# Performance work log

Hardware: AMD Instinct MI355X
Metric: run time of the kernel (lower is better)

Reference implementation:

```python
import jax, jax.numpy as jnp
import numpy as np

EPS = 1e-5
GROUPS = 32


def group_norm(x, w, b):
    # x: [N, C]; GroupNorm over 1x1 spatial == per-group norm over C//GROUPS chans
    N, C = x.shape
    xg = x.reshape(N, GROUPS, C // GROUPS)
    mu = xg.mean(-1, keepdims=True)
    var = xg.var(-1, keepdims=True)
    xn = ((xg - mu) * jax.lax.rsqrt(var + EPS)).reshape(N, C)
    return xn * w + b


def rb(x, gn1w, gn1b, c1w, c1b, gn2w, gn2b, c2w, c2b):
    # Conv2d 3x3 pad=1 on a 1x1 spatial input: only the center tap sees data
    # (all other taps hit zero padding), so it reduces exactly to a GEMM with
    # the [out, in] center slice of the kernel.
    h = jax.nn.silu(group_norm(x, gn1w, gn1b))
    h = h @ c1w[:, :, 1, 1].T + c1b
    h = jax.nn.silu(group_norm(h, gn2w, gn2b))
    h = h @ c2w[:, :, 1, 1].T + c2b
    return h + x  # skip == Identity (in_ch == out_ch)


def setup_inputs() -> dict:
    key = jax.random.key(0)
    ks = jax.random.split(key, 20)
    BS, CAND, D, H, W = 32, 2048, 256, 32, 32
    s = 0.05
    inp = {
        "gimage": jax.random.normal(ks[0], (BS, D, H, W), dtype=jnp.float32),
        "pts": jax.random.randint(ks[1], (BS, CAND, 1, 2), 0, 256, dtype=jnp.int32),
        # two stacked RB blocks
        "gn1_w": jnp.ones((2, D), jnp.float32),
        "gn1_b": jnp.zeros((2, D), jnp.float32),
        "conv1_w": jax.random.normal(ks[2], (2, D, D, 3, 3), jnp.float32) * s,
        "conv1_b": jnp.zeros((2, D), jnp.float32),
        "gn2_w": jnp.ones((2, D), jnp.float32),
        "gn2_b": jnp.zeros((2, D), jnp.float32),
        "conv2_w": jax.random.normal(ks[3], (2, D, D, 3, 3), jnp.float32) * s,
        "conv2_b": jnp.zeros((2, D), jnp.float32),
        # class_embed: Linear(256, 2)
        "cls_w": jax.random.normal(ks[4], (2, D), jnp.float32) * s,
        "cls_b": jnp.zeros((2,), jnp.float32),
        # bbox_embed: MLP(256, 256, 4, 3)
        "mlp_w1": jax.random.normal(ks[5], (D, D), jnp.float32) * s,
        "mlp_b1": jnp.zeros((D,), jnp.float32),
        "mlp_w2": jax.random.normal(ks[6], (D, D), jnp.float32) * s,
        "mlp_b2": jnp.zeros((D,), jnp.float32),
        "mlp_w3": jax.random.normal(ks[7], (4, D), jnp.float32) * s,
        "mlp_b3": jnp.zeros((4,), jnp.float32),
    }
    return inp


def reference(gimage, pts, gn1_w, gn1_b, conv1_w, conv1_b, gn2_w, gn2_b,
              conv2_w, conv2_b, cls_w, cls_b, mlp_w1, mlp_b1, mlp_w2, mlp_b2,
              mlp_w3, mlp_b3):
    bs, C, H, W = gimage.shape
    c = pts.shape[1]
    # patch_idx = (pts // 8)[:, :, 0, :] -> (iy, ix) per (batch, candidate)
    idx = pts[:, :, 0, :] // 8                      # [bs, c, 2]
    lin = idx[..., 0] * W + idx[..., 1]             # [bs, c] flat spatial index
    g = gimage.reshape(bs, C, H * W)
    feat = jnp.take_along_axis(g, lin[:, None, :].astype(jnp.int32), axis=2)  # [bs, C, c]
    x = feat.transpose(0, 2, 1).reshape(bs * c, C)  # [(bs c), 256]

    for i in range(2):  # convLayer = Sequential(RB, RB)
        x = rb(x, gn1_w[i], gn1_b[i], conv1_w[i], conv1_b[i],
               gn2_w[i], gn2_b[i], conv2_w[i], conv2_b[i])

    logits = x @ cls_w.T + cls_b                    # [(bs c), 2]
    h = jax.nn.relu(x @ mlp_w1.T + mlp_b1)
    h = jax.nn.relu(h @ mlp_w2.T + mlp_b2)
    boxes = jax.nn.sigmoid(h @ mlp_w3.T + mlp_b3)   # [(bs c), 4]

    pred_logits = logits.reshape(bs, c, 2)
    pred_boxes = boxes.reshape(bs, c, 4)
    return pred_logits, pred_boxes
```

## Files before the change

### kernel.cpp

```cpp
#include <hip/hip_runtime.h>


typedef __attribute__((ext_vector_type(8))) _Float16 half8;
typedef __attribute__((ext_vector_type(4))) float f32x4;

#define AS 264

#define NHALF  393216
#define OFF_WC1 0
#define OFF_WC2 131072
#define OFF_W1  262144
#define OFF_W2  327680
#define WS_NEED 1572864

__device__ __forceinline__ float sigm(float y) { return 1.f / (1.f + __expf(-y)); }

__global__ __launch_bounds__(256) void prep(const float* __restrict__ c1w,
                                            const float* __restrict__ c2w,
                                            const float* __restrict__ w1,
                                            const float* __restrict__ w2,
                                            _Float16* __restrict__ ws) {
  int i = blockIdx.x * 256 + threadIdx.x;
  {
    float v = c1w[(size_t)i * 9 + 4];
    _Float16 h = (_Float16)v;
    ws[OFF_WC1 + i] = h;
    ws[NHALF + OFF_WC1 + i] = (_Float16)(v - (float)h);
  }
  {
    float v = c2w[(size_t)i * 9 + 4];
    _Float16 h = (_Float16)v;
    ws[OFF_WC2 + i] = h;
    ws[NHALF + OFF_WC2 + i] = (_Float16)(v - (float)h);
  }
  if (i < 65536) {
    float v = w1[i];
    _Float16 h = (_Float16)v;
    ws[OFF_W1 + i] = h;
    ws[NHALF + OFF_W1 + i] = (_Float16)(v - (float)h);
    v = w2[i];
    h = (_Float16)v;
    ws[OFF_W2 + i] = h;
    ws[NHALF + OFF_W2 + i] = (_Float16)(v - (float)h);
  }
}

__device__ __forceinline__ void hl_store(_Float16* __restrict__ Ah,
                                         _Float16* __restrict__ Al,
                                         int idx, float v) {
  _Float16 h = (_Float16)v;
  Ah[idx] = h;
  Al[idx] = (_Float16)(v - (float)h);
}

__device__ __forceinline__ void mfma_run(f32x4 acc[2][4],
    const _Float16* __restrict__ Ah, const _Float16* __restrict__ Al,
    const _Float16* __restrict__ Wh, const _Float16* __restrict__ Wl,
    int aoff, size_t boff) {
  half8 bh[4], bl[4];
  #pragma unroll
  for (int nt = 0; nt < 4; nt++) {
    bh[nt] = *(const half8*)(Wh + boff + (nt << 12));
    bl[nt] = *(const half8*)(Wl + boff + (nt << 12));
  }
  #pragma unroll
  for (int mt = 0; mt < 2; mt++)
    #pragma unroll
    for (int nt = 0; nt < 4; nt++)
      acc[mt][nt] = (f32x4){0.f, 0.f, 0.f, 0.f};
  __syncthreads();
  #pragma unroll
  for (int kt = 0; kt < 8; kt++) {
    half8 ah0 = *(const half8*)(Ah + aoff + kt * 32);
    half8 ah1 = *(const half8*)(Ah + aoff + 16 * AS + kt * 32);
    half8 al0 = *(const half8*)(Al + aoff + kt * 32);
    half8 al1 = *(const half8*)(Al + aoff + 16 * AS + kt * 32);
    #pragma unroll
    for (int nt = 0; nt < 4; nt++) {
      acc[0][nt] = __builtin_amdgcn_mfma_f32_16x16x32_f16(ah0, bh[nt], acc[0][nt], 0, 0, 0);
      acc[1][nt] = __builtin_amdgcn_mfma_f32_16x16x32_f16(ah1, bh[nt], acc[1][nt], 0, 0, 0);
      acc[0][nt] = __builtin_amdgcn_mfma_f32_16x16x32_f16(ah0, bl[nt], acc[0][nt], 0, 0, 0);
      acc[1][nt] = __builtin_amdgcn_mfma_f32_16x16x32_f16(ah1, bl[nt], acc[1][nt], 0, 0, 0);
      acc[0][nt] = __builtin_amdgcn_mfma_f32_16x16x32_f16(al0, bh[nt], acc[0][nt], 0, 0, 0);
      acc[1][nt] = __builtin_amdgcn_mfma_f32_16x16x32_f16(al1, bh[nt], acc[1][nt], 0, 0, 0);
    }
    if (kt < 7) {
      #pragma unroll
      for (int nt = 0; nt < 4; nt++) {
        bh[nt] = *(const half8*)(Wh + boff + (nt << 12) + (kt + 1) * 32);
        bl[nt] = *(const half8*)(Wl + boff + (nt << 12) + (kt + 1) * 32);
      }
    }
  }
}

__device__ __forceinline__ void gn_x_to_A(const float x[2][4][4],
    const float* __restrict__ gnw, const float* __restrict__ gnb,
    int col, int quad, int nb,
    _Float16* __restrict__ Ah, _Float16* __restrict__ Al) {
  #pragma unroll
  for (int nt = 0; nt < 4; nt++) {
    int n = nb + (nt << 4) + col;
    float gwv = gnw[n], gbv = gnb[n];
    #pragma unroll
    for (int mt = 0; mt < 2; mt++) {
      #pragma unroll
      for (int rg = 0; rg < 4; rg++) {
        float v = x[mt][nt][rg];
        float s = v, q = v * v;
        s += __shfl_xor(s, 1); q += __shfl_xor(q, 1);
        s += __shfl_xor(s, 2); q += __shfl_xor(q, 2);
        s += __shfl_xor(s, 4); q += __shfl_xor(q, 4);
        float mu = s * 0.125f;
        float rs = rsqrtf(q * 0.125f - mu * mu + 1e-5f);
        float y = (v - mu) * rs * gwv + gbv;
        float sv = y * sigm(y);
        hl_store(Ah, Al, ((mt << 4) + (quad << 2) + rg) * AS + n, sv);
      }
    }
  }
}

__device__ __forceinline__ void epi_gn_to_A(const f32x4 acc[2][4],
    const float* __restrict__ bias,
    const float* __restrict__ gnw, const float* __restrict__ gnb,
    int col, int quad, int nb,
    _Float16* __restrict__ Ah, _Float16* __restrict__ Al) {
  #pragma unroll
  for (int nt = 0; nt < 4; nt++) {
    int n = nb + (nt << 4) + col;
    float bv = bias[n];
    float gwv = gnw[n], gbv = gnb[n];
    #pragma unroll
    for (int mt = 0; mt < 2; mt++) {
      #pragma unroll
      for (int rg = 0; rg < 4; rg++) {
        float v = acc[mt][nt][rg] + bv;
        float s = v, q = v * v;
        s += __shfl_xor(s, 1); q += __shfl_xor(q, 1);
        s += __shfl_xor(s, 2); q += __shfl_xor(q, 2);
        s += __shfl_xor(s, 4); q += __shfl_xor(q, 4);
        float mu = s * 0.125f;
        float rs = rsqrtf(q * 0.125f - mu * mu + 1e-5f);
        float y = (v - mu) * rs * gwv + gbv;
        float sv = y * sigm(y);
        hl_store(Ah, Al, ((mt << 4) + (quad << 2) + rg) * AS + n, sv);
      }
    }
  }
}

__device__ __forceinline__ void epi_relu_to_A(const f32x4 acc[2][4],
    const float* __restrict__ bias, int col, int quad, int nb,
    _Float16* __restrict__ Ah, _Float16* __restrict__ Al) {
  #pragma unroll
  for (int nt = 0; nt < 4; nt++) {
    int n = nb + (nt << 4) + col;
    float bv = bias[n];
    #pragma unroll
    for (int mt = 0; mt < 2; mt++)
      #pragma unroll
      for (int rg = 0; rg < 4; rg++)
        hl_store(Ah, Al, ((mt << 4) + (quad << 2) + rg) * AS + n,
                 fmaxf(acc[mt][nt][rg] + bv, 0.f));
  }
}

__global__ __launch_bounds__(256, 4) void fused_mfma(
    const float* __restrict__ gimage, const int* __restrict__ pts,
    const float* __restrict__ gn1w, const float* __restrict__ gn1b,
    const float* __restrict__ c1b,
    const float* __restrict__ gn2w, const float* __restrict__ gn2b,
    const float* __restrict__ c2b,
    const float* __restrict__ clsw, const float* __restrict__ clsb,
    const float* __restrict__ b1, const float* __restrict__ b2,
    const float* __restrict__ w3, const float* __restrict__ b3,
    const _Float16* __restrict__ ws, float* __restrict__ out) {
  __shared__ _Float16 Ah[32 * AS];
  __shared__ _Float16 Al[32 * AS];
  __shared__ float red[4][32][4];

  const int t = threadIdx.x;
  const int w = t >> 6;
  const int lane = t & 63;
  const int col = lane & 15;
  const int quad = lane >> 4;
  const int nb = w << 6;
  const int row0 = blockIdx.x << 5;
  const int rbase = quad << 2;

  const int aoff = col * AS + (quad << 3);
  const size_t boff = (((size_t)(nb + col)) << 8) + (quad << 3);
  const _Float16* wsl = ws + NHALF;

  float x[2][4][4];
  {
    int lin[2][4];
    #pragma unroll
    for (int mt = 0; mt < 2; mt++)
      #pragma unroll
      for (int rg = 0; rg < 4; rg++) {
        int grow = row0 + (mt << 4) + rbase + rg;
        int p0 = pts[2 * grow], p1 = pts[2 * grow + 1];
        lin[mt][rg] = ((p0 >> 3) << 5) + (p1 >> 3);
      }
    const float* gbase = gimage + (((size_t)((row0 >> 11) << 8)) << 10);
    #pragma unroll
    for (int nt = 0; nt < 4; nt++) {
      const float* gc = gbase + (((size_t)(nb + (nt << 4) + col)) << 10);
      #pragma unroll
      for (int mt = 0; mt < 2; mt++)
        #pragma unroll
        for (int rg = 0; rg < 4; rg++)
          x[mt][nt][rg] = gc[lin[mt][rg]];
    }
  }

  f32x4 acc[2][4];

  #pragma unroll 1
  for (int rb = 0; rb < 2; rb++) {
    gn_x_to_A(x, gn1w + (rb << 8), gn1b + (rb << 8), col, quad, nb, Ah, Al);
    mfma_run(acc, Ah, Al, ws + OFF_WC1 + (rb << 16), wsl + OFF_WC1 + (rb << 16),
             aoff, boff);
    __syncthreads();
    epi_gn_to_A(acc, c1b + (rb << 8), gn2w + (rb << 8), gn2b + (rb << 8),
                col, quad, nb, Ah, Al);
    mfma_run(acc, Ah, Al, ws + OFF_WC2 + (rb << 16), wsl + OFF_WC2 + (rb << 16),
             aoff, boff);
    __syncthreads();
    #pragma unroll
    for (int nt = 0; nt < 4; nt++) {
      float bv = c2b[(rb << 8) + nb + (nt << 4) + col];
      #pragma unroll
      for (int mt = 0; mt < 2; mt++)
        #pragma unroll
        for (int rg = 0; rg < 4; rg++)
          x[mt][nt][rg] += acc[mt][nt][rg] + bv;
    }
  }

  #pragma unroll
  for (int nt = 0; nt < 4; nt++) {
    int n = nb + (nt << 4) + col;
    #pragma unroll
    for (int mt = 0; mt < 2; mt++)
      #pragma unroll
      for (int rg = 0; rg < 4; rg++)
        hl_store(Ah, Al, ((mt << 4) + rbase + rg) * AS + n, x[mt][nt][rg]);
  }
  {
    float pc[2][2][4];
    #pragma unroll
    for (int j = 0; j < 2; j++) {
      #pragma unroll
      for (int mt = 0; mt < 2; mt++)
        #pragma unroll
        for (int rg = 0; rg < 4; rg++)
          pc[j][mt][rg] = 0.f;
      #pragma unroll
      for (int nt = 0; nt < 4; nt++) {
        float wv = clsw[(j << 8) + nb + (nt << 4) + col];
        #pragma unroll
        for (int mt = 0; mt < 2; mt++)
          #pragma unroll
          for (int rg = 0; rg < 4; rg++)
            pc[j][mt][rg] += x[mt][nt][rg] * wv;
      }
    }
    #pragma unroll
    for (int j = 0; j < 2; j++)
      #pragma unroll
      for (int mt = 0; mt < 2; mt++)
        #pragma unroll
        for (int rg = 0; rg < 4; rg++) {
          float p = pc[j][mt][rg];
          p += __shfl_xor(p, 1);
          p += __shfl_xor(p, 2);
          p += __shfl_xor(p, 4);
          p += __shfl_xor(p, 8);
          if (col == 0) red[w][(mt << 4) + rbase + rg][j] = p;
        }
  }

  mfma_run(acc, Ah, Al, ws + OFF_W1, wsl + OFF_W1, aoff, boff);
  if (t < 64) {
    int r = t >> 1, j = t & 1;
    out[((size_t)(row0 + r) << 1) + j] =
        clsb[j] + red[0][r][j] + red[1][r][j] + red[2][r][j] + red[3][r][j];
  }
  __syncthreads();
  epi_relu_to_A(acc, b1, col, quad, nb, Ah, Al);

  mfma_run(acc, Ah, Al, ws + OFF_W2, wsl + OFF_W2, aoff, boff);
  __syncthreads();
  {
    float pb[4][2][4];
    #pragma unroll
    for (int j = 0; j < 4; j++)
      #pragma unroll
      for (int mt = 0; mt < 2; mt++)
        #pragma unroll
        for (int rg = 0; rg < 4; rg++)
          pb[j][mt][rg] = 0.f;
    #pragma unroll
    for (int nt = 0; nt < 4; nt++) {
      int n = nb + (nt << 4) + col;
      float bv = b2[n];
      float w0 = w3[n], w1v = w3[256 + n], w2v = w3[512 + n], w3v = w3[768 + n];
      #pragma unroll
      for (int mt = 0; mt < 2; mt++)
        #pragma unroll
        for (int rg = 0; rg < 4; rg++) {
          float v = fmaxf(acc[mt][nt][rg] + bv, 0.f);
          pb[0][mt][rg] += v * w0;
          pb[1][mt][rg] += v * w1v;
          pb[2][mt][rg] += v * w2v;
          pb[3][mt][rg] += v * w3v;
        }
    }
    #pragma unroll
    for (int j = 0; j < 4; j++)
      #pragma unroll
      for (int mt = 0; mt < 2; mt++)
        #pragma unroll
        for (int rg = 0; rg < 4; rg++) {
          float p = pb[j][mt][rg];
          p += __shfl_xor(p, 1);
          p += __shfl_xor(p, 2);
          p += __shfl_xor(p, 4);
          p += __shfl_xor(p, 8);
          if (col == 0) red[w][(mt << 4) + rbase + rg][j] = p;
        }
  }
  __syncthreads();
  if (t < 128) {
    int r = t >> 2, j = t & 3;
    float s = b3[j] + red[0][r][j] + red[1][r][j] + red[2][r][j] + red[3][r][j];
    out[131072 + ((size_t)(row0 + r) << 2) + j] = sigm(s);
  }
}

#define LS 260
template <int EPI, bool CONV>
__device__ __forceinline__ void gemm_f32(const float* __restrict__ src,
                                         const float* __restrict__ W,
                                         const float* __restrict__ bias,
                                         float* __restrict__ dst,
                                         float* __restrict__ X) {
  const int n = threadIdx.x;
  float acc[32];
  #pragma unroll
  for (int r = 0; r < 32; r++) acc[r] = 0.f;
  #pragma unroll 1
  for (int k = 0; k < 256; k += 8) {
    float w[8];
    if (CONV) {
      #pragma unroll
      for (int j = 0; j < 8; j++) w[j] = W[(size_t)((n << 8) + k + j) * 9 + 4];
    } else {
      f32x4 wa = *(const f32x4*)(W + (n << 8) + k);
      f32x4 wb = *(const f32x4*)(W + (n << 8) + k + 4);
      w[0] = wa[0]; w[1] = wa[1]; w[2] = wa[2]; w[3] = wa[3];
      w[4] = wb[0]; w[5] = wb[1]; w[6] = wb[2]; w[7] = wb[3];
    }
    #pragma unroll
    for (int r = 0; r < 32; r++) {
      const float* xr = src + r * LS + k;
      f32x4 a0 = *(const f32x4*)xr, a1 = *(const f32x4*)(xr + 4);
      acc[r] += a0[0] * w[0] + a0[1] * w[1] + a0[2] * w[2] + a0[3] * w[3]
              + a1[0] * w[4] + a1[1] * w[5] + a1[2] * w[6] + a1[3] * w[7];
    }
  }
  float bv = bias[n];
  #pragma unroll
  for (int r = 0; r < 32; r++) {
    float v = acc[r] + bv;
    if (EPI == 0) dst[r * LS + n] = v;
    else if (EPI == 1) X[r * LS + n] += v;
    else dst[r * LS + n] = fmaxf(v, 0.f);
  }
}
__device__ __forceinline__ void gn_silu32(const float* __restrict__ src,
                                          float* __restrict__ dst,
                                          const float* __restrict__ gw,
                                          const float* __restrict__ gb, int t) {
  #pragma unroll
  for (int i = 0; i < 4; i++) {
    int task = (i << 8) + t;
    int r = task >> 5, g = task & 31;
    const float* x = src + r * LS + (g << 3);
    f32x4 x0 = *(const f32x4*)x, x1 = *(const f32x4*)(x + 4);
    float xx[8] = {x0[0], x0[1], x0[2], x0[3], x1[0], x1[1], x1[2], x1[3]};
    float s = 0.f, q = 0.f;
    #pragma unroll
    for (int j = 0; j < 8; j++) { s += xx[j]; q += xx[j] * xx[j]; }
    float mu = s * 0.125f;
    float rs = rsqrtf(q * 0.125f - mu * mu + 1e-5f);
    const float* w = gw + (g << 3);
    const float* b = gb + (g << 3);
    float* d = dst + r * LS + (g << 3);
    #pragma unroll
    for (int j = 0; j < 8; j++) {
      float y = (xx[j] - mu) * rs * w[j] + b[j];
      d[j] = y * sigm(y);
    }
  }
}
__global__ __launch_bounds__(256, 1) void fused_all(
    const float* __restrict__ gimage, const int* __restrict__ pts,
    const float* __restrict__ gn1w, const float* __restrict__ gn1b,
    const float* __restrict__ c1w, const float* __restrict__ c1b,
    const float* __restrict__ gn2w, const float* __restrict__ gn2b,
    const float* __restrict__ c2w, const float* __restrict__ c2b,
    const float* __restrict__ clsw, const float* __restrict__ clsb,
    const float* __restrict__ w1, const float* __restrict__ b1,
    const float* __restrict__ w2, const float* __restrict__ b2,
    const float* __restrict__ w3, const float* __restrict__ b3,
    float* __restrict__ out) {
  __shared__ float X[32 * LS];
  __shared__ float A[32 * LS];
  __shared__ float H[32 * LS];
  const int t = threadIdx.x;
  const int row0 = blockIdx.x << 5;
  {
    int r = t >> 3;
    int c0 = (t & 7) << 5;
    int grow = row0 + r;
    int p0 = pts[2 * grow], p1 = pts[2 * grow + 1];
    int lin = ((p0 >> 3) << 5) + (p1 >> 3);
    int b = grow >> 11;
    const float* src = gimage + (((size_t)((b << 8) + c0)) << 10) + lin;
    #pragma unroll
    for (int c = 0; c < 32; c++) X[r * LS + c0 + c] = src[(size_t)c << 10];
  }
  __syncthreads();
  #pragma unroll 1
  for (int rb = 0; rb < 2; rb++) {
    gn_silu32(X, A, gn1w + (rb << 8), gn1b + (rb << 8), t);
    __syncthreads();
    gemm_f32<0, true>(A, c1w + rb * 589824, c1b + (rb << 8), H, nullptr);
    __syncthreads();
    gn_silu32(H, A, gn2w + (rb << 8), gn2b + (rb << 8), t);
    __syncthreads();
    gemm_f32<1, true>(A, c2w + rb * 589824, c2b + (rb << 8), nullptr, X);
    __syncthreads();
  }
  if (t < 64) {
    int r = t >> 1, j = t & 1;
    float s = clsb[j];
    const float* w = clsw + (j << 8);
    const float* x = X + r * LS;
    #pragma unroll 1
    for (int k = 0; k < 256; k += 4) {
      f32x4 wv = *(const f32x4*)(w + k);
      f32x4 xv = *(const f32x4*)(x + k);
      s += xv[0] * wv[0] + xv[1] * wv[1] + xv[2] * wv[2] + xv[3] * wv[3];
    }
    out[((size_t)(row0 + r) << 1) + j] = s;
  }
  gemm_f32<2, false>(X, w1, b1, H, nullptr);
  __syncthreads();
  gemm_f32<2, false>(H, w2, b2, A, nullptr);
  __syncthreads();
  if (t < 128) {
    int r = t >> 2, j = t & 3;
    float s = b3[j];
    const float* w = w3 + (j << 8);
    const float* x = A + r * LS;
    #pragma unroll 1
    for (int k = 0; k < 256; k += 4) {
      f32x4 wv = *(const f32x4*)(w + k);
      f32x4 xv = *(const f32x4*)(x + k);
      s += xv[0] * wv[0] + xv[1] * wv[1] + xv[2] * wv[2] + xv[3] * wv[3];
    }
    out[131072 + ((size_t)(row0 + r) << 2) + j] = sigm(s);
  }
}

extern "C" void kernel_launch(void* const* d_in, const int* in_sizes, int n_in,
                              void* d_out, int out_size, void* d_ws, size_t ws_size,
                              hipStream_t stream) {
  const float* gimage = (const float*)d_in[0];
  const int* pts = (const int*)d_in[1];
  const float* gn1w = (const float*)d_in[2];
  const float* gn1b = (const float*)d_in[3];
  const float* c1w = (const float*)d_in[4];
  const float* c1b = (const float*)d_in[5];
  const float* gn2w = (const float*)d_in[6];
  const float* gn2b = (const float*)d_in[7];
  const float* c2w = (const float*)d_in[8];
  const float* c2b = (const float*)d_in[9];
  const float* clsw = (const float*)d_in[10];
  const float* clsb = (const float*)d_in[11];
  const float* w1 = (const float*)d_in[12];
  const float* b1 = (const float*)d_in[13];
  const float* w2 = (const float*)d_in[14];
  const float* b2 = (const float*)d_in[15];
  const float* w3 = (const float*)d_in[16];
  const float* b3 = (const float*)d_in[17];

  if (ws_size >= (size_t)WS_NEED) {
    _Float16* ws = (_Float16*)d_ws;
    prep<<<512, 256, 0, stream>>>(c1w, c2w, w1, w2, ws);
    fused_mfma<<<2048, 256, 0, stream>>>(gimage, pts, gn1w, gn1b, c1b,
                                         gn2w, gn2b, c2b, clsw, clsb,
                                         b1, b2, w3, b3, ws, (float*)d_out);
  } else {
    fused_all<<<2048, 256, 0, stream>>>(gimage, pts, gn1w, gn1b, c1w, c1b,
                                        gn2w, gn2b, c2w, c2b, clsw, clsb,
                                        w1, b1, w2, b2, w3, b3, (float*)d_out);
  }
}
```

Baseline: 548.5 us.

## Double rows per block to 64 with 512 threads sharing weight fragments

```diff
diff --git a/kernel.cpp b/kernel.cpp
--- a/kernel.cpp
+++ b/kernel.cpp
@@ -96,7 +96,7 @@
 
 __device__ __forceinline__ void gn_x_to_A(const float x[2][4][4],
     const float* __restrict__ gnw, const float* __restrict__ gnb,
-    int col, int quad, int nb,
+    int col, int quad, int nb, int rh,
     _Float16* __restrict__ Ah, _Float16* __restrict__ Al) {
   #pragma unroll
   for (int nt = 0; nt < 4; nt++) {
@@ -115,7 +115,7 @@
         float rs = rsqrtf(q * 0.125f - mu * mu + 1e-5f);
         float y = (v - mu) * rs * gwv + gbv;
         float sv = y * sigm(y);
-        hl_store(Ah, Al, ((mt << 4) + (quad << 2) + rg) * AS + n, sv);
+        hl_store(Ah, Al, (rh + (mt << 4) + (quad << 2) + rg) * AS + n, sv);
       }
     }
   }
@@ -124,7 +124,7 @@
 __device__ __forceinline__ void epi_gn_to_A(const f32x4 acc[2][4],
     const float* __restrict__ bias,
     const float* __restrict__ gnw, const float* __restrict__ gnb,
-    int col, int quad, int nb,
+    int col, int quad, int nb, int rh,
     _Float16* __restrict__ Ah, _Float16* __restrict__ Al) {
   #pragma unroll
   for (int nt = 0; nt < 4; nt++) {
@@ -144,14 +144,14 @@
         float rs = rsqrtf(q * 0.125f - mu * mu + 1e-5f);
         float y = (v - mu) * rs * gwv + gbv;
         float sv = y * sigm(y);
-        hl_store(Ah, Al, ((mt << 4) + (quad << 2) + rg) * AS + n, sv);
+        hl_store(Ah, Al, (rh + (mt << 4) + (quad << 2) + rg) * AS + n, sv);
       }
     }
   }
 }
 
 __device__ __forceinline__ void epi_relu_to_A(const f32x4 acc[2][4],
-    const float* __restrict__ bias, int col, int quad, int nb,
+    const float* __restrict__ bias, int col, int quad, int nb, int rh,
     _Float16* __restrict__ Ah, _Float16* __restrict__ Al) {
   #pragma unroll
   for (int nt = 0; nt < 4; nt++) {
@@ -161,12 +161,12 @@
     for (int mt = 0; mt < 2; mt++)
       #pragma unroll
       for (int rg = 0; rg < 4; rg++)
-        hl_store(Ah, Al, ((mt << 4) + (quad << 2) + rg) * AS + n,
+        hl_store(Ah, Al, (rh + (mt << 4) + (quad << 2) + rg) * AS + n,
                  fmaxf(acc[mt][nt][rg] + bv, 0.f));
   }
 }
 
-__global__ __launch_bounds__(256, 4) void fused_mfma(
+__global__ __launch_bounds__(512, 3) void fused_mfma(
     const float* __restrict__ gimage, const int* __restrict__ pts,
     const float* __restrict__ gn1w, const float* __restrict__ gn1b,
     const float* __restrict__ c1b,
@@ -176,20 +176,21 @@
     const float* __restrict__ b1, const float* __restrict__ b2,
     const float* __restrict__ w3, const float* __restrict__ b3,
     const _Float16* __restrict__ ws, float* __restrict__ out) {
-  __shared__ _Float16 Ah[32 * AS];
-  __shared__ _Float16 Al[32 * AS];
-  __shared__ float red[4][32][4];
+  __shared__ _Float16 Ah[64 * AS];
+  __shared__ _Float16 Al[64 * AS];
+  __shared__ float red[8][32][4];
 
   const int t = threadIdx.x;
   const int w = t >> 6;
   const int lane = t & 63;
   const int col = lane & 15;
   const int quad = lane >> 4;
-  const int nb = w << 6;
-  const int row0 = blockIdx.x << 5;
+  const int nb = (w & 3) << 6;
+  const int rh = (w >> 2) << 5;
+  const int row0 = blockIdx.x << 6;
   const int rbase = quad << 2;
 
-  const int aoff = col * AS + (quad << 3);
+  const int aoff = (rh + col) * AS + (quad << 3);
   const size_t boff = (((size_t)(nb + col)) << 8) + (quad << 3);
   const _Float16* wsl = ws + NHALF;
 
@@ -200,7 +201,7 @@
     for (int mt = 0; mt < 2; mt++)
       #pragma unroll
       for (int rg = 0; rg < 4; rg++) {
-        int grow = row0 + (mt << 4) + rbase + rg;
+        int grow = row0 + rh + (mt << 4) + rbase + rg;
         int p0 = pts[2 * grow], p1 = pts[2 * grow + 1];
         lin[mt][rg] = ((p0 >> 3) << 5) + (p1 >> 3);
       }
@@ -220,12 +221,12 @@
 
   #pragma unroll 1
   for (int rb = 0; rb < 2; rb++) {
-    gn_x_to_A(x, gn1w + (rb << 8), gn1b + (rb << 8), col, quad, nb, Ah, Al);
+    gn_x_to_A(x, gn1w + (rb << 8), gn1b + (rb << 8), col, quad, nb, rh, Ah, Al);
     mfma_run(acc, Ah, Al, ws + OFF_WC1 + (rb << 16), wsl + OFF_WC1 + (rb << 16),
              aoff, boff);
     __syncthreads();
     epi_gn_to_A(acc, c1b + (rb << 8), gn2w + (rb << 8), gn2b + (rb << 8),
-                col, quad, nb, Ah, Al);
+                col, quad, nb, rh, Ah, Al);
     mfma_run(acc, Ah, Al, ws + OFF_WC2 + (rb << 16), wsl + OFF_WC2 + (rb << 16),
              aoff, boff);
     __syncthreads();
@@ -247,7 +248,7 @@
     for (int mt = 0; mt < 2; mt++)
       #pragma unroll
       for (int rg = 0; rg < 4; rg++)
-        hl_store(Ah, Al, ((mt << 4) + rbase + rg) * AS + n, x[mt][nt][rg]);
+        hl_store(Ah, Al, (rh + (mt << 4) + rbase + rg) * AS + n, x[mt][nt][rg]);
   }
   {
     float pc[2][2][4];
@@ -284,13 +285,15 @@
   }
 
   mfma_run(acc, Ah, Al, ws + OFF_W1, wsl + OFF_W1, aoff, boff);
-  if (t < 64) {
+  if (t < 128) {
     int r = t >> 1, j = t & 1;
+    int h = (r >> 5) << 2, lr = r & 31;
     out[((size_t)(row0 + r) << 1) + j] =
-        clsb[j] + red[0][r][j] + red[1][r][j] + red[2][r][j] + red[3][r][j];
-  }
-  __syncthreads();
-  epi_relu_to_A(acc, b1, col, quad, nb, Ah, Al);
+        clsb[j] + red[h][lr][j] + red[h + 1][lr][j] + red[h + 2][lr][j] +
+        red[h + 3][lr][j];
+  }
+  __syncthreads();
+  epi_relu_to_A(acc, b1, col, quad, nb, rh, Ah, Al);
 
   mfma_run(acc, Ah, Al, ws + OFF_W2, wsl + OFF_W2, aoff, boff);
   __syncthreads();
@@ -334,9 +337,11 @@
         }
   }
   __syncthreads();
-  if (t < 128) {
+  if (t < 256) {
     int r = t >> 2, j = t & 3;
-    float s = b3[j] + red[0][r][j] + red[1][r][j] + red[2][r][j] + red[3][r][j];
+    int h = (r >> 5) << 2, lr = r & 31;
+    float s = b3[j] + red[h][lr][j] + red[h + 1][lr][j] + red[h + 2][lr][j] +
+              red[h + 3][lr][j];
     out[131072 + ((size_t)(row0 + r) << 2) + j] = sigm(s);
   }
 }
@@ -503,7 +508,7 @@
   if (ws_size >= (size_t)WS_NEED) {
     _Float16* ws = (_Float16*)d_ws;
     prep<<<512, 256, 0, stream>>>(c1w, c2w, w1, w2, ws);
-    fused_mfma<<<2048, 256, 0, stream>>>(gimage, pts, gn1w, gn1b, c1b,
+    fused_mfma<<<1024, 512, 0, stream>>>(gimage, pts, gn1w, gn1b, c1b,
                                          gn2w, gn2b, c2b, clsw, clsb,
                                          b1, b2, w3, b3, ws, (float*)d_out);
   } else {
```

Measured after the change: 660.3 us. 1.2x slower.
